# Kernel tuning notes

Hardware: AMD Instinct MI355X
Metric: run time of the kernel (lower is better)

The kernel has to match this reference:

```python
import jax, jax.numpy as jnp
import numpy as np

N, E, F, HID, HEADS, G = 20000, 320000, 64, 64, 4, 64
HC = HEADS * HID  # 256
NHID, NOUT = 256, 128
INV_SQRT2 = 0.7071067811865476


def _gat(x, src, dst, W, a_s, a_d, bias):
    # GATConv (v1), eval mode (no dropout); src/dst already include self-loops (PyG default)
    H, C = a_s.shape
    h = (x @ W).reshape(-1, H, C)  # [N,H,C]
    al_s = jnp.einsum('nhc,hc->nh', h, a_s)
    al_d = jnp.einsum('nhc,hc->nh', h, a_d)
    e = jax.nn.leaky_relu(al_s[src] + al_d[dst], 0.2)  # [Etot,H]
    m = jax.ops.segment_max(e, dst, num_segments=N)
    ex = jnp.exp(e - m[dst])
    den = jax.ops.segment_sum(ex, dst, num_segments=N)
    coef = ex / den[dst]  # softmax over incoming edges per target node
    out = jax.ops.segment_sum(h[src] * coef[:, :, None], dst, num_segments=N)
    return out.reshape(-1, H * C) + bias


def _bn(h, g, b):
    # BatchNorm1d, training-mode stats (biased var), eps=1e-5
    mu = h.mean(axis=0)
    var = h.var(axis=0)
    return g * (h - mu) * jax.lax.rsqrt(var + 1e-5) + b


def _block(x, src, dst, W1, a1s, a1d, b1, g1, be1, W2, a2s, a2d, b2, g2, be2, Wr, br, Wf, bf):
    h = jax.nn.relu(_bn(_gat(x, src, dst, W1, a1s, a1d, b1), g1, be1))
    h = jax.nn.relu(_bn(_gat(h, src, dst, W2, a2s, a2d, b2), g2, be2))
    res = x @ Wr + br
    return ((h + res) * INV_SQRT2) @ Wf + bf


def setup_inputs():
    ks = iter(jax.random.split(jax.random.key(0), 64))
    def rn(shape, scale=0.05):
        return jax.random.normal(next(ks), shape, dtype=jnp.float32) * scale
    inp = {}
    inp['x'] = jax.random.normal(next(ks), (N, F), dtype=jnp.float32)
    inp['edge_index'] = jax.random.randint(next(ks), (2, E), 0, N, dtype=jnp.int32)
    inp['batch'] = jnp.sort(jax.random.randint(next(ks), (N,), 0, G, dtype=jnp.int32))
    for b, cin in enumerate([F, HID]):
        p = 'b%d_' % b
        inp[p + 'W1'] = rn((cin, HC)); inp[p + 'a1s'] = rn((HEADS, HID)); inp[p + 'a1d'] = rn((HEADS, HID))
        inp[p + 'b1'] = jnp.zeros((HC,), jnp.float32)
        inp[p + 'g1'] = jnp.ones((HC,), jnp.float32); inp[p + 'be1'] = jnp.zeros((HC,), jnp.float32)
        inp[p + 'W2'] = rn((HC, HC)); inp[p + 'a2s'] = rn((1, HC)); inp[p + 'a2d'] = rn((1, HC))
        inp[p + 'b2'] = jnp.zeros((HC,), jnp.float32)
        inp[p + 'g2'] = jnp.ones((HC,), jnp.float32); inp[p + 'be2'] = jnp.zeros((HC,), jnp.float32)
        inp[p + 'Wr'] = rn((cin, HC)); inp[p + 'br'] = jnp.zeros((HC,), jnp.float32)
        inp[p + 'Wf'] = rn((HC, HID)); inp[p + 'bf'] = jnp.zeros((HID,), jnp.float32)
    inp['Wh1'] = rn((HID, NHID)); inp['bh1'] = jnp.zeros((NHID,), jnp.float32)
    inp['Wh2'] = rn((NHID, NOUT)); inp['bh2'] = jnp.zeros((NOUT,), jnp.float32)
    return inp


def reference(x, edge_index, batch,
              b0_W1, b0_a1s, b0_a1d, b0_b1, b0_g1, b0_be1, b0_W2, b0_a2s, b0_a2d, b0_b2, b0_g2, b0_be2, b0_Wr, b0_br, b0_Wf, b0_bf,
              b1_W1, b1_a1s, b1_a1d, b1_b1, b1_g1, b1_be1, b1_W2, b1_a2s, b1_a2d, b1_b2, b1_g2, b1_be2, b1_Wr, b1_br, b1_Wf, b1_bf,
              Wh1, bh1, Wh2, bh2):
    loops = jnp.arange(N, dtype=edge_index.dtype)
    src = jnp.concatenate([edge_index[0], loops])
    dst = jnp.concatenate([edge_index[1], loops])
    x = _block(x, src, dst, b0_W1, b0_a1s, b0_a1d, b0_b1, b0_g1, b0_be1, b0_W2, b0_a2s, b0_a2d, b0_b2, b0_g2, b0_be2, b0_Wr, b0_br, b0_Wf, b0_bf)
    x = _block(x, src, dst, b1_W1, b1_a1s, b1_a1d, b1_b1, b1_g1, b1_be1, b1_W2, b1_a2s, b1_a2d, b1_b2, b1_g2, b1_be2, b1_Wr, b1_br, b1_Wf, b1_bf)
    cnt = jax.ops.segment_sum(jnp.ones((N,), x.dtype), batch, num_segments=G)
    pooled = jax.ops.segment_sum(x, batch, num_segments=G) / jnp.maximum(cnt, 1.0)[:, None]
    h = jax.nn.relu(pooled @ Wh1 + bh1)
    return h @ Wh2 + bh2
```

## Files before the change

kernel.cpp:

```cpp
#include <hip/hip_runtime.h>

#define N_NODES 20000
#define N_EDGES 320000
#define ETOT (N_EDGES + N_NODES)
#define G_GROUPS 64


__global__ __launch_bounds__(256) void k_hist(const int* __restrict__ ei, int* __restrict__ counts) {
    int e = blockIdx.x * 256 + threadIdx.x;
    if (e >= ETOT) return;
    int dst = (e < N_EDGES) ? ei[N_EDGES + e] : (e - N_EDGES);
    atomicAdd(&counts[dst], 1);
}

__global__ __launch_bounds__(1024) void k_scan(const int* __restrict__ counts, int* __restrict__ offs,
                                               int* __restrict__ cursor) {
    __shared__ int sdata[1024];
    const int t = threadIdx.x;
    const int chunk = (N_NODES + 1023) / 1024;
    int base = t * chunk;
    int s = 0;
    for (int i = 0; i < chunk; i++) { int idx = base + i; if (idx < N_NODES) s += counts[idx]; }
    sdata[t] = s;
    __syncthreads();
    for (int off = 1; off < 1024; off <<= 1) {
        int v = (t >= off) ? sdata[t - off] : 0;
        __syncthreads();
        sdata[t] += v;
        __syncthreads();
    }
    int prefix = (t == 0) ? 0 : sdata[t - 1];
    for (int i = 0; i < chunk; i++) {
        int idx = base + i;
        if (idx < N_NODES) {
            int cv = counts[idx];
            offs[idx] = prefix;
            cursor[idx] = prefix;
            prefix += cv;
        }
    }
    if (t == 1023) offs[N_NODES] = sdata[1023];
}

__global__ __launch_bounds__(256) void k_scatter(const int* __restrict__ ei, int* __restrict__ cursor,
                                                 int* __restrict__ csr_src, int* __restrict__ csr_dst) {
    int e = blockIdx.x * 256 + threadIdx.x;
    if (e >= ETOT) return;
    int src = (e < N_EDGES) ? ei[e] : (e - N_EDGES);
    int dst = (e < N_EDGES) ? ei[N_EDGES + e] : (e - N_EDGES);
    int p = atomicAdd(&cursor[dst], 1);
    csr_src[p] = src;
    csr_dst[p] = dst;
}


template <int H>
__global__ __launch_bounds__(256) void k_edgew(const int* __restrict__ csr_src, const int* __restrict__ csr_dst,
                                               const float* __restrict__ alS, const float* __restrict__ alD,
                                               float* __restrict__ wex) {
    int p = blockIdx.x * 256 + threadIdx.x;
    if (p >= ETOT) return;
    int s = csr_src[p], d = csr_dst[p];
    if (H == 4) {
        float4 a = *(const float4*)(alS + s * 4);
        float4 b = *(const float4*)(alD + d * 4);
        float4 v = {a.x + b.x, a.y + b.y, a.z + b.z, a.w + b.w};
        v.x = (v.x > 0.f) ? v.x : 0.2f * v.x;
        v.y = (v.y > 0.f) ? v.y : 0.2f * v.y;
        v.z = (v.z > 0.f) ? v.z : 0.2f * v.z;
        v.w = (v.w > 0.f) ? v.w : 0.2f * v.w;
        float4 w = {__expf(v.x), __expf(v.y), __expf(v.z), __expf(v.w)};
        *(float4*)(wex + p * 4) = w;
    } else {
        float v = alS[s] + alD[d];
        v = (v > 0.f) ? v : 0.2f * v;
        wex[p] = __expf(v);
    }
}


__global__ __launch_bounds__(256) void k_gemm64_dual(const float* __restrict__ x, const float* __restrict__ W1,
                                                     const float* __restrict__ Wr, const float* __restrict__ br,
                                                     const float* __restrict__ a_s, const float* __restrict__ a_d,
                                                     float* __restrict__ h, float* __restrict__ res,
                                                     float* __restrict__ alS, float* __restrict__ alD) {
    const int rb = blockIdx.x >> 2, cs = blockIdx.x & 3;
    const int row0 = rb * 64;
    const int nrows = min(64, N_NODES - row0);
    const int t = threadIdx.x;
    __shared__ float xs[32 * 68];
    __shared__ float b1s[32 * 64];
    __shared__ float brs[32 * 64];
    const int lane = t & 63;
    const int c0 = (t & 15) * 4;
    const int r0 = (t >> 4) * 4;
    const int rl = (t & 15) | ((t >> 6) << 4);
    const int c4 = (t >> 4) & 3;
    float acc1[4][4] = {}, acc2[4][4] = {};
    for (int k0 = 0; k0 < 64; k0 += 32) {
        if (k0) __syncthreads();
        {
            #pragma unroll
            for (int jj = 0; jj < 2; jj++) {
                int cc = c4 + 4 * jj;
                float4 v = {0.f, 0.f, 0.f, 0.f};
                if (rl < nrows) v = *(const float4*)(x + (row0 + rl) * 64 + k0 + cc * 4);
                xs[(cc * 4 + 0) * 68 + rl] = v.x;
                xs[(cc * 4 + 1) * 68 + rl] = v.y;
                xs[(cc * 4 + 2) * 68 + rl] = v.z;
                xs[(cc * 4 + 3) * 68 + rl] = v.w;
            }
        }
        {
            int cc = (t & 15) * 4;
            int k = t >> 4;
            #pragma unroll
            for (int pass = 0; pass < 2; pass++, k += 16) {
                *(float4*)(b1s + k * 64 + cc) = *(const float4*)(W1 + (k0 + k) * 256 + cs * 64 + cc);
                *(float4*)(brs + k * 64 + cc) = *(const float4*)(Wr + (k0 + k) * 256 + cs * 64 + cc);
            }
        }
        __syncthreads();
        #pragma unroll 8
        for (int k = 0; k < 32; k++) {
            float4 av = *(const float4*)(xs + k * 68 + r0);
            float4 b1 = *(const float4*)(b1s + k * 64 + c0);
            float4 b2 = *(const float4*)(brs + k * 64 + c0);
            float a[4] = {av.x, av.y, av.z, av.w};
            #pragma unroll
            for (int i = 0; i < 4; i++) {
                acc1[i][0] += a[i] * b1.x; acc1[i][1] += a[i] * b1.y;
                acc1[i][2] += a[i] * b1.z; acc1[i][3] += a[i] * b1.w;
                acc2[i][0] += a[i] * b2.x; acc2[i][1] += a[i] * b2.y;
                acc2[i][2] += a[i] * b2.z; acc2[i][3] += a[i] * b2.w;
            }
        }
    }
    const int gcol = cs * 64 + c0;
    float4 bv = *(const float4*)(br + gcol);
    float4 asv = *(const float4*)(a_s + gcol);
    float4 adv = *(const float4*)(a_d + gcol);
    #pragma unroll
    for (int i = 0; i < 4; i++) {
        int gr = row0 + r0 + i;
        bool ok = (r0 + i) < nrows;
        float4 o1 = {acc1[i][0], acc1[i][1], acc1[i][2], acc1[i][3]};
        if (ok) {
            *(float4*)(h + gr * 256 + gcol) = o1;
            float4 o2 = {acc2[i][0] + bv.x, acc2[i][1] + bv.y, acc2[i][2] + bv.z, acc2[i][3] + bv.w};
            *(float4*)(res + gr * 256 + gcol) = o2;
        }
        float ps = o1.x * asv.x + o1.y * asv.y + o1.z * asv.z + o1.w * asv.w;
        float pd = o1.x * adv.x + o1.y * adv.y + o1.z * adv.z + o1.w * adv.w;
        #pragma unroll
        for (int off = 8; off > 0; off >>= 1) {
            ps += __shfl_down(ps, off);
            pd += __shfl_down(pd, off);
        }
        if (((lane & 15) == 0) && ok) {
            alS[gr * 4 + cs] = ps;
            alD[gr * 4 + cs] = pd;
        }
    }
}


__global__ __launch_bounds__(256) void k_alpha(const float* __restrict__ h, const float* __restrict__ a_s,
                                               const float* __restrict__ a_d, float* __restrict__ alS,
                                               float* __restrict__ alD) {
    int node = blockIdx.x * 4 + (threadIdx.x >> 6);
    int lane = threadIdx.x & 63;
    if (node >= N_NODES) return;
    const float4 hv = *(const float4*)(h + node * 256 + lane * 4);
    const float4 as = *(const float4*)(a_s + lane * 4);
    const float4 ad = *(const float4*)(a_d + lane * 4);
    float ps = hv.x * as.x + hv.y * as.y + hv.z * as.z + hv.w * as.w;
    float pd = hv.x * ad.x + hv.y * ad.y + hv.z * ad.z + hv.w * ad.w;
    #pragma unroll
    for (int off = 32; off > 0; off >>= 1) {
        ps += __shfl_down(ps, off);
        pd += __shfl_down(pd, off);
    }
    if (lane == 0) {
        alS[node] = ps;
        alD[node] = pd;
    }
}


template <int H>
__global__ __launch_bounds__(256) void k_agg(const float* __restrict__ h, const float* __restrict__ wex,
                                             const int* __restrict__ offs, const int* __restrict__ csr_src,
                                             const float* __restrict__ bias, float* __restrict__ out) {
    int node = blockIdx.x * 4 + (threadIdx.x >> 6);
    int lane = threadIdx.x & 63;
    if (node >= N_NODES) return;
    const int head = (lane * H) >> 6;
    int e0 = offs[node], e1 = offs[node + 1];
    float den = 0.f, a0 = 0.f, a1 = 0.f, a2 = 0.f, a3 = 0.f;
    int e = e0;
    for (; e + 4 <= e1; e += 4) {
        int s0 = csr_src[e], s1 = csr_src[e + 1], s2 = csr_src[e + 2], s3 = csr_src[e + 3];
        float w0 = wex[(e + 0) * H + head];
        float w1 = wex[(e + 1) * H + head];
        float w2 = wex[(e + 2) * H + head];
        float w3 = wex[(e + 3) * H + head];
        const float4 h0 = *(const float4*)(h + s0 * 256 + lane * 4);
        const float4 h1 = *(const float4*)(h + s1 * 256 + lane * 4);
        const float4 h2 = *(const float4*)(h + s2 * 256 + lane * 4);
        const float4 h3 = *(const float4*)(h + s3 * 256 + lane * 4);
        den += (w0 + w1) + (w2 + w3);
        a0 += w0 * h0.x + w1 * h1.x + w2 * h2.x + w3 * h3.x;
        a1 += w0 * h0.y + w1 * h1.y + w2 * h2.y + w3 * h3.y;
        a2 += w0 * h0.z + w1 * h1.z + w2 * h2.z + w3 * h3.z;
        a3 += w0 * h0.w + w1 * h1.w + w2 * h2.w + w3 * h3.w;
    }
    for (; e < e1; e++) {
        int s = csr_src[e];
        float w = wex[e * H + head];
        const float4 hv = *(const float4*)(h + s * 256 + lane * 4);
        den += w;
        a0 += w * hv.x; a1 += w * hv.y; a2 += w * hv.z; a3 += w * hv.w;
    }
    float inv = 1.f / den;
    const float4 bv = *(const float4*)(bias + lane * 4);
    float4 o = {a0 * inv + bv.x, a1 * inv + bv.y, a2 * inv + bv.z, a3 * inv + bv.w};
    *(float4*)(out + node * 256 + lane * 4) = o;
}


__global__ __launch_bounds__(256) void k_bnstats(const float* __restrict__ x, float* __restrict__ sum,
                                                 float* __restrict__ sumsq) {
    int c = threadIdx.x;
    float s = 0.f, q = 0.f;
    for (int r = blockIdx.x; r < N_NODES; r += gridDim.x) {
        float v = x[r * 256 + c];
        s += v; q += v * v;
    }
    atomicAdd(&sum[c], s);
    atomicAdd(&sumsq[c], q);
}

__global__ __launch_bounds__(256) void k_bnfin(const float* __restrict__ sum, const float* __restrict__ sumsq,
                                               const float* __restrict__ g, const float* __restrict__ be,
                                               float* __restrict__ scale, float* __restrict__ shift) {
    int c = threadIdx.x;
    float mu = sum[c] * (1.f / N_NODES);
    float var = sumsq[c] * (1.f / N_NODES) - mu * mu;
    float sc = g[c] * rsqrtf(var + 1e-5f);
    scale[c] = sc;
    shift[c] = be[c] - mu * sc;
}


__global__ __launch_bounds__(256) void k_gemm256(const float* __restrict__ A, const float* __restrict__ scale,
                                                 const float* __restrict__ shift, const float* __restrict__ B,
                                                 float* __restrict__ C) {
    const int rb = blockIdx.x >> 2, cs = blockIdx.x & 3;
    const int row0 = rb * 128;
    const int col0 = cs * 64;
    const int nrows = min(128, N_NODES - row0);
    const int t = threadIdx.x;
    __shared__ float xs[32 * 132];
    __shared__ float bs[32 * 64];
    __shared__ float scs[256], shs[256];
    scs[t] = scale[t];
    shs[t] = shift[t];
    const int rl = (t & 15) | ((t >> 6) << 4);
    const int c4 = (t >> 4) & 3;
    const int c0 = (t & 15) * 4;
    const int r0 = (t >> 4) * 8;
    float acc[8][4] = {};
    for (int k0 = 0; k0 < 256; k0 += 32) {
        __syncthreads();
        #pragma unroll
        for (int i = 0; i < 2; i++) {
            int r = rl + 64 * i;
            #pragma unroll
            for (int jj = 0; jj < 2; jj++) {
                int cc = c4 + 4 * jj;
                int kcol = k0 + cc * 4;
                float4 w = {0.f, 0.f, 0.f, 0.f};
                if (r < nrows) {
                    float4 v = *(const float4*)(A + (row0 + r) * 256 + kcol);
                    w.x = fmaxf(v.x * scs[kcol + 0] + shs[kcol + 0], 0.f);
                    w.y = fmaxf(v.y * scs[kcol + 1] + shs[kcol + 1], 0.f);
                    w.z = fmaxf(v.z * scs[kcol + 2] + shs[kcol + 2], 0.f);
                    w.w = fmaxf(v.w * scs[kcol + 3] + shs[kcol + 3], 0.f);
                }
                xs[(cc * 4 + 0) * 132 + r] = w.x;
                xs[(cc * 4 + 1) * 132 + r] = w.y;
                xs[(cc * 4 + 2) * 132 + r] = w.z;
                xs[(cc * 4 + 3) * 132 + r] = w.w;
            }
        }
        {
            int ccB = (t & 15) * 4;
            int kB = t >> 4;
            #pragma unroll
            for (int pass = 0; pass < 2; pass++, kB += 16) {
                *(float4*)(bs + kB * 64 + ccB) = *(const float4*)(B + (k0 + kB) * 256 + col0 + ccB);
            }
        }
        __syncthreads();
        #pragma unroll 8
        for (int k = 0; k < 32; k++) {
            float4 a0 = *(const float4*)(xs + k * 132 + r0);
            float4 a1 = *(const float4*)(xs + k * 132 + r0 + 4);
            float4 bv = *(const float4*)(bs + k * 64 + c0);
            float a[8] = {a0.x, a0.y, a0.z, a0.w, a1.x, a1.y, a1.z, a1.w};
            #pragma unroll
            for (int i = 0; i < 8; i++) {
                acc[i][0] += a[i] * bv.x; acc[i][1] += a[i] * bv.y;
                acc[i][2] += a[i] * bv.z; acc[i][3] += a[i] * bv.w;
            }
        }
    }
    #pragma unroll
    for (int i = 0; i < 8; i++) {
        if ((r0 + i) < nrows) {
            int gr = row0 + r0 + i;
            float4 o = {acc[i][0], acc[i][1], acc[i][2], acc[i][3]};
            *(float4*)(C + gr * 256 + col0 + c0) = o;
        }
    }
}


__global__ __launch_bounds__(256) void k_gemm_final(const float* __restrict__ A, const float* __restrict__ scale,
                                                    const float* __restrict__ shift, const float* __restrict__ res,
                                                    const float* __restrict__ B, const float* __restrict__ bias,
                                                    float* __restrict__ y) {
    const int row0 = blockIdx.x * 32;
    const int t = threadIdx.x;
    const float INVS = 0.70710678118654752440f;
    __shared__ float xs[32 * 36];
    __shared__ float bs[32 * 64];
    __shared__ float scs[256], shs[256];
    scs[t] = scale[t];
    shs[t] = shift[t];
    const int rf = (t & 15) | ((t >> 7) << 4);
    const int cf = (t >> 4) & 7;
    const int c0 = (t & 15) * 4;
    const int r0 = (t >> 4) * 2;
    float acc[2][4] = {};
    for (int k0 = 0; k0 < 256; k0 += 32) {
        __syncthreads();
        {
            int kcol = k0 + cf * 4;
            int gi = (row0 + rf) * 256 + kcol;
            float4 v = *(const float4*)(A + gi);
            float4 rv = *(const float4*)(res + gi);
            xs[(cf * 4 + 0) * 36 + rf] = (fmaxf(v.x * scs[kcol + 0] + shs[kcol + 0], 0.f) + rv.x) * INVS;
            xs[(cf * 4 + 1) * 36 + rf] = (fmaxf(v.y * scs[kcol + 1] + shs[kcol + 1], 0.f) + rv.y) * INVS;
            xs[(cf * 4 + 2) * 36 + rf] = (fmaxf(v.z * scs[kcol + 2] + shs[kcol + 2], 0.f) + rv.z) * INVS;
            xs[(cf * 4 + 3) * 36 + rf] = (fmaxf(v.w * scs[kcol + 3] + shs[kcol + 3], 0.f) + rv.w) * INVS;
        }
        {
            int cc = (t & 15) * 4;
            int k = t >> 4;
            #pragma unroll
            for (int pass = 0; pass < 2; pass++, k += 16) {
                *(float4*)(bs + k * 64 + cc) = *(const float4*)(B + (k0 + k) * 64 + cc);
            }
        }
        __syncthreads();
        #pragma unroll 8
        for (int k = 0; k < 32; k++) {
            float2 av = *(const float2*)(xs + k * 36 + r0);
            float4 bv = *(const float4*)(bs + k * 64 + c0);
            acc[0][0] += av.x * bv.x; acc[0][1] += av.x * bv.y;
            acc[0][2] += av.x * bv.z; acc[0][3] += av.x * bv.w;
            acc[1][0] += av.y * bv.x; acc[1][1] += av.y * bv.y;
            acc[1][2] += av.y * bv.z; acc[1][3] += av.y * bv.w;
        }
    }
    float4 bv = *(const float4*)(bias + c0);
    #pragma unroll
    for (int i = 0; i < 2; i++) {
        int gr = row0 + r0 + i;
        float4 o = {acc[i][0] + bv.x, acc[i][1] + bv.y, acc[i][2] + bv.z, acc[i][3] + bv.w};
        *(float4*)(y + gr * 64 + c0) = o;
    }
}


__global__ __launch_bounds__(256) void k_pool_head(const float* __restrict__ x, const int* __restrict__ batch,
                                                   const float* __restrict__ Wh1, const float* __restrict__ bh1,
                                                   const float* __restrict__ Wh2, const float* __restrict__ bh2,
                                                   float* __restrict__ out) {
    const int g = blockIdx.x;
    const int t = threadIdx.x;
    int lo = 0, hi = N_NODES;
    while (lo < hi) { int mid = (lo + hi) >> 1; if (batch[mid] < g) lo = mid + 1; else hi = mid; }
    int start = lo;
    hi = N_NODES;
    while (lo < hi) { int mid = (lo + hi) >> 1; if (batch[mid] < g + 1) lo = mid + 1; else hi = mid; }
    int end = lo;
    float cnt = (float)(end - start);

    __shared__ float part[256];
    __shared__ float p[64];
    __shared__ float hrow[256];
    const int c = t & 63;
    float s = 0.f;
    for (int r = start + (t >> 6); r < end; r += 4) s += x[r * 64 + c];
    part[t] = s;
    __syncthreads();
    if (t < 64) {
        float v = part[t] + part[t + 64] + part[t + 128] + part[t + 192];
        p[t] = v / fmaxf(cnt, 1.f);
    }
    __syncthreads();
    float a = bh1[t];
    #pragma unroll 8
    for (int k = 0; k < 64; k++) a += p[k] * Wh1[k * 256 + t];
    hrow[t] = fmaxf(a, 0.f);
    __syncthreads();
    if (t < 128) {
        float o = bh2[t];
        #pragma unroll 8
        for (int k = 0; k < 256; k++) o += hrow[k] * Wh2[k * 128 + t];
        out[g * 128 + t] = o;
    }
}


extern "C" void kernel_launch(void* const* d_in, const int* in_sizes, int n_in,
                              void* d_out, int out_size, void* d_ws, size_t ws_size,
                              hipStream_t stream) {
    (void)in_sizes; (void)n_in; (void)out_size; (void)ws_size;
    const float* x0 = (const float*)d_in[0];
    const int* ei = (const int*)d_in[1];
    const int* batch = (const int*)d_in[2];
    const float* Wh1 = (const float*)d_in[35];
    const float* bh1 = (const float*)d_in[36];
    const float* Wh2 = (const float*)d_in[37];
    const float* bh2 = (const float*)d_in[38];

    char* p = (char*)d_ws;
    auto alloc = [&](size_t bytes) -> void* {
        void* r = (void*)p;
        p += (bytes + 255) & ~(size_t)255;
        return r;
    };
    int* counts = (int*)alloc((size_t)N_NODES * 4);
    int* offs = (int*)alloc((size_t)(N_NODES + 1) * 4);
    int* cursor = (int*)alloc((size_t)N_NODES * 4);
    int* csr_src = (int*)alloc((size_t)ETOT * 4);
    int* csr_dst = (int*)alloc((size_t)ETOT * 4);
    float* wex = (float*)alloc((size_t)ETOT * 4 * 4);
    float* alS = (float*)alloc((size_t)N_NODES * 4 * 4);
    float* alD = (float*)alloc((size_t)N_NODES * 4 * 4);
    float* bnsum = (float*)alloc(2048);
    float* bnsq = bnsum + 256;
    float* scaleb = (float*)alloc(1024);
    float* shiftb = (float*)alloc(1024);
    float* hbuf = (float*)alloc((size_t)N_NODES * 256 * 4);
    float* obuf = (float*)alloc((size_t)N_NODES * 256 * 4);
    float* rbuf = (float*)alloc((size_t)N_NODES * 256 * 4);
    float* xout = (float*)alloc((size_t)N_NODES * 64 * 4);

    hipMemsetAsync(counts, 0, (size_t)N_NODES * 4, stream);
    k_hist<<<(ETOT + 255) / 256, 256, 0, stream>>>(ei, counts);
    k_scan<<<1, 1024, 0, stream>>>(counts, offs, cursor);
    k_scatter<<<(ETOT + 255) / 256, 256, 0, stream>>>(ei, cursor, csr_src, csr_dst);

    const int tile64_blocks = ((N_NODES + 63) / 64) * 4;
    const int tile128_blocks = ((N_NODES + 127) / 128) * 4;
    const int node_blocks = (N_NODES + 3) / 4;
    const int edge_blocks = (ETOT + 255) / 256;
    const int final_blocks = N_NODES / 32;

    auto run_block = [&](const float* xin, int base) {
        const float* W1 = (const float*)d_in[base + 0];
        const float* a1s = (const float*)d_in[base + 1];
        const float* a1d = (const float*)d_in[base + 2];
        const float* b1 = (const float*)d_in[base + 3];
        const float* g1 = (const float*)d_in[base + 4];
        const float* be1 = (const float*)d_in[base + 5];
        const float* W2 = (const float*)d_in[base + 6];
        const float* a2s = (const float*)d_in[base + 7];
        const float* a2d = (const float*)d_in[base + 8];
        const float* b2 = (const float*)d_in[base + 9];
        const float* g2 = (const float*)d_in[base + 10];
        const float* be2 = (const float*)d_in[base + 11];
        const float* Wr = (const float*)d_in[base + 12];
        const float* br = (const float*)d_in[base + 13];
        const float* Wf = (const float*)d_in[base + 14];
        const float* bf = (const float*)d_in[base + 15];

        k_gemm64_dual<<<tile64_blocks, 256, 0, stream>>>(xin, W1, Wr, br, a1s, a1d, hbuf, rbuf, alS, alD);
        k_edgew<4><<<edge_blocks, 256, 0, stream>>>(csr_src, csr_dst, alS, alD, wex);
        k_agg<4><<<node_blocks, 256, 0, stream>>>(hbuf, wex, offs, csr_src, b1, obuf);
        hipMemsetAsync(bnsum, 0, 2048, stream);
        k_bnstats<<<256, 256, 0, stream>>>(obuf, bnsum, bnsq);
        k_bnfin<<<1, 256, 0, stream>>>(bnsum, bnsq, g1, be1, scaleb, shiftb);
        k_gemm256<<<tile128_blocks, 256, 0, stream>>>(obuf, scaleb, shiftb, W2, hbuf);
        k_alpha<<<node_blocks, 256, 0, stream>>>(hbuf, a2s, a2d, alS, alD);
        k_edgew<1><<<edge_blocks, 256, 0, stream>>>(csr_src, csr_dst, alS, alD, wex);
        k_agg<1><<<node_blocks, 256, 0, stream>>>(hbuf, wex, offs, csr_src, b2, obuf);
        hipMemsetAsync(bnsum, 0, 2048, stream);
        k_bnstats<<<256, 256, 0, stream>>>(obuf, bnsum, bnsq);
        k_bnfin<<<1, 256, 0, stream>>>(bnsum, bnsq, g2, be2, scaleb, shiftb);
        k_gemm_final<<<final_blocks, 256, 0, stream>>>(obuf, scaleb, shiftb, rbuf, Wf, bf, xout);
    };

    run_block(x0, 3);
    run_block(xout, 19);

    k_pool_head<<<G_GROUPS, 256, 0, stream>>>(xout, batch, Wh1, bh1, Wh2, bh2, (float*)d_out);
}
```

Measured before the change: 738.7 us.

## Fuse edge softmax weights into aggregation and alpha into second GEMM

Attention edge weights are now computed inside the aggregation kernel from per-node alpha values, which removes the separate edge-weight kernels, the wex buffer and csr_dst. The second-layer alpha dot products are folded into the 256-wide GEMM epilogue as per-column-slice partials, summed by a small reduction kernel, so the standalone alpha kernel goes away. That GEMM's row tile drops from 128 to 64, and the BN accumulators are zeroed by k_bnfin and the initial memset instead of per-layer memsets. The aggregation loop is unrolled by 8 edges, at the cost of extra exp work and alpha gathers per lane.

New measurement: 705.7 us. 1.05x faster.

```diff
diff --git a/kernel.cpp b/kernel.cpp
--- a/kernel.cpp
+++ b/kernel.cpp
@@ -43,39 +43,13 @@
 }
 
 __global__ __launch_bounds__(256) void k_scatter(const int* __restrict__ ei, int* __restrict__ cursor,
-                                                 int* __restrict__ csr_src, int* __restrict__ csr_dst) {
+                                                 int* __restrict__ csr_src) {
     int e = blockIdx.x * 256 + threadIdx.x;
     if (e >= ETOT) return;
     int src = (e < N_EDGES) ? ei[e] : (e - N_EDGES);
     int dst = (e < N_EDGES) ? ei[N_EDGES + e] : (e - N_EDGES);
     int p = atomicAdd(&cursor[dst], 1);
     csr_src[p] = src;
-    csr_dst[p] = dst;
-}
-
-
-template <int H>
-__global__ __launch_bounds__(256) void k_edgew(const int* __restrict__ csr_src, const int* __restrict__ csr_dst,
-                                               const float* __restrict__ alS, const float* __restrict__ alD,
-                                               float* __restrict__ wex) {
-    int p = blockIdx.x * 256 + threadIdx.x;
-    if (p >= ETOT) return;
-    int s = csr_src[p], d = csr_dst[p];
-    if (H == 4) {
-        float4 a = *(const float4*)(alS + s * 4);
-        float4 b = *(const float4*)(alD + d * 4);
-        float4 v = {a.x + b.x, a.y + b.y, a.z + b.z, a.w + b.w};
-        v.x = (v.x > 0.f) ? v.x : 0.2f * v.x;
-        v.y = (v.y > 0.f) ? v.y : 0.2f * v.y;
-        v.z = (v.z > 0.f) ? v.z : 0.2f * v.z;
-        v.w = (v.w > 0.f) ? v.w : 0.2f * v.w;
-        float4 w = {__expf(v.x), __expf(v.y), __expf(v.z), __expf(v.w)};
-        *(float4*)(wex + p * 4) = w;
-    } else {
-        float v = alS[s] + alD[d];
-        v = (v > 0.f) ? v : 0.2f * v;
-        wex[p] = __expf(v);
-    }
 }
 
 
@@ -165,60 +139,47 @@
 }
 
 
-__global__ __launch_bounds__(256) void k_alpha(const float* __restrict__ h, const float* __restrict__ a_s,
-                                               const float* __restrict__ a_d, float* __restrict__ alS,
-                                               float* __restrict__ alD) {
+template <int H>
+__global__ __launch_bounds__(256) void k_agg(const float* __restrict__ h, const float* __restrict__ alS,
+                                             const float* __restrict__ alD, const int* __restrict__ offs,
+                                             const int* __restrict__ csr_src, const float* __restrict__ bias,
+                                             float* __restrict__ out) {
     int node = blockIdx.x * 4 + (threadIdx.x >> 6);
     int lane = threadIdx.x & 63;
     if (node >= N_NODES) return;
-    const float4 hv = *(const float4*)(h + node * 256 + lane * 4);
-    const float4 as = *(const float4*)(a_s + lane * 4);
-    const float4 ad = *(const float4*)(a_d + lane * 4);
-    float ps = hv.x * as.x + hv.y * as.y + hv.z * as.z + hv.w * as.w;
-    float pd = hv.x * ad.x + hv.y * ad.y + hv.z * ad.z + hv.w * ad.w;
-    #pragma unroll
-    for (int off = 32; off > 0; off >>= 1) {
-        ps += __shfl_down(ps, off);
-        pd += __shfl_down(pd, off);
-    }
-    if (lane == 0) {
-        alS[node] = ps;
-        alD[node] = pd;
-    }
-}
-
-
-template <int H>
-__global__ __launch_bounds__(256) void k_agg(const float* __restrict__ h, const float* __restrict__ wex,
-                                             const int* __restrict__ offs, const int* __restrict__ csr_src,
-                                             const float* __restrict__ bias, float* __restrict__ out) {
-    int node = blockIdx.x * 4 + (threadIdx.x >> 6);
-    int lane = threadIdx.x & 63;
-    if (node >= N_NODES) return;
-    const int head = (lane * H) >> 6;
+    const int head = (H == 4) ? (lane >> 4) : 0;
+    const float ald = alD[node * H + head];
     int e0 = offs[node], e1 = offs[node + 1];
+    const float* hp = h + lane * 4;
     float den = 0.f, a0 = 0.f, a1 = 0.f, a2 = 0.f, a3 = 0.f;
     int e = e0;
-    for (; e + 4 <= e1; e += 4) {
-        int s0 = csr_src[e], s1 = csr_src[e + 1], s2 = csr_src[e + 2], s3 = csr_src[e + 3];
-        float w0 = wex[(e + 0) * H + head];
-        float w1 = wex[(e + 1) * H + head];
-        float w2 = wex[(e + 2) * H + head];
-        float w3 = wex[(e + 3) * H + head];
-        const float4 h0 = *(const float4*)(h + s0 * 256 + lane * 4);
-        const float4 h1 = *(const float4*)(h + s1 * 256 + lane * 4);
-        const float4 h2 = *(const float4*)(h + s2 * 256 + lane * 4);
-        const float4 h3 = *(const float4*)(h + s3 * 256 + lane * 4);
-        den += (w0 + w1) + (w2 + w3);
-        a0 += w0 * h0.x + w1 * h1.x + w2 * h2.x + w3 * h3.x;
-        a1 += w0 * h0.y + w1 * h1.y + w2 * h2.y + w3 * h3.y;
-        a2 += w0 * h0.z + w1 * h1.z + w2 * h2.z + w3 * h3.z;
-        a3 += w0 * h0.w + w1 * h1.w + w2 * h2.w + w3 * h3.w;
+    for (; e + 8 <= e1; e += 8) {
+        int s[8];
+        #pragma unroll
+        for (int i = 0; i < 8; i++) s[i] = csr_src[e + i];
+        float4 hv[8];
+        #pragma unroll
+        for (int i = 0; i < 8; i++) hv[i] = *(const float4*)(hp + s[i] * 256);
+        float w[8];
+        #pragma unroll
+        for (int i = 0; i < 8; i++) {
+            float v = alS[s[i] * H + head] + ald;
+            v = (v > 0.f) ? v : 0.2f * v;
+            w[i] = __expf(v);
+        }
+        #pragma unroll
+        for (int i = 0; i < 8; i++) {
+            den += w[i];
+            a0 += w[i] * hv[i].x; a1 += w[i] * hv[i].y;
+            a2 += w[i] * hv[i].z; a3 += w[i] * hv[i].w;
+        }
     }
     for (; e < e1; e++) {
         int s = csr_src[e];
-        float w = wex[e * H + head];
-        const float4 hv = *(const float4*)(h + s * 256 + lane * 4);
+        float v = alS[s * H + head] + ald;
+        v = (v > 0.f) ? v : 0.2f * v;
+        float w = __expf(v);
+        const float4 hv = *(const float4*)(hp + s * 256);
         den += w;
         a0 += w * hv.x; a1 += w * hv.y; a2 += w * hv.z; a3 += w * hv.w;
     }
@@ -241,7 +202,7 @@
     atomicAdd(&sumsq[c], q);
 }
 
-__global__ __launch_bounds__(256) void k_bnfin(const float* __restrict__ sum, const float* __restrict__ sumsq,
+__global__ __launch_bounds__(256) void k_bnfin(float* __restrict__ sum, float* __restrict__ sumsq,
                                                const float* __restrict__ g, const float* __restrict__ be,
                                                float* __restrict__ scale, float* __restrict__ shift) {
     int c = threadIdx.x;
@@ -250,48 +211,51 @@
     float sc = g[c] * rsqrtf(var + 1e-5f);
     scale[c] = sc;
     shift[c] = be[c] - mu * sc;
+    sum[c] = 0.f;
+    sumsq[c] = 0.f;
 }
 
 
 __global__ __launch_bounds__(256) void k_gemm256(const float* __restrict__ A, const float* __restrict__ scale,
                                                  const float* __restrict__ shift, const float* __restrict__ B,
-                                                 float* __restrict__ C) {
+                                                 const float* __restrict__ a_s, const float* __restrict__ a_d,
+                                                 float* __restrict__ C, float* __restrict__ alSp,
+                                                 float* __restrict__ alDp) {
     const int rb = blockIdx.x >> 2, cs = blockIdx.x & 3;
-    const int row0 = rb * 128;
+    const int row0 = rb * 64;
     const int col0 = cs * 64;
-    const int nrows = min(128, N_NODES - row0);
+    const int nrows = min(64, N_NODES - row0);
     const int t = threadIdx.x;
-    __shared__ float xs[32 * 132];
+    __shared__ float xs[32 * 68];
     __shared__ float bs[32 * 64];
     __shared__ float scs[256], shs[256];
     scs[t] = scale[t];
     shs[t] = shift[t];
+    const int lane = t & 63;
     const int rl = (t & 15) | ((t >> 6) << 4);
     const int c4 = (t >> 4) & 3;
     const int c0 = (t & 15) * 4;
-    const int r0 = (t >> 4) * 8;
-    float acc[8][4] = {};
+    const int r0 = (t >> 4) * 4;
+    float acc[4][4] = {};
     for (int k0 = 0; k0 < 256; k0 += 32) {
         __syncthreads();
-        #pragma unroll
-        for (int i = 0; i < 2; i++) {
-            int r = rl + 64 * i;
+        {
             #pragma unroll
             for (int jj = 0; jj < 2; jj++) {
                 int cc = c4 + 4 * jj;
                 int kcol = k0 + cc * 4;
                 float4 w = {0.f, 0.f, 0.f, 0.f};
-                if (r < nrows) {
-                    float4 v = *(const float4*)(A + (row0 + r) * 256 + kcol);
+                if (rl < nrows) {
+                    float4 v = *(const float4*)(A + (row0 + rl) * 256 + kcol);
                     w.x = fmaxf(v.x * scs[kcol + 0] + shs[kcol + 0], 0.f);
                     w.y = fmaxf(v.y * scs[kcol + 1] + shs[kcol + 1], 0.f);
                     w.z = fmaxf(v.z * scs[kcol + 2] + shs[kcol + 2], 0.f);
                     w.w = fmaxf(v.w * scs[kcol + 3] + shs[kcol + 3], 0.f);
                 }
-                xs[(cc * 4 + 0) * 132 + r] = w.x;
-                xs[(cc * 4 + 1) * 132 + r] = w.y;
-                xs[(cc * 4 + 2) * 132 + r] = w.z;
-                xs[(cc * 4 + 3) * 132 + r] = w.w;
+                xs[(cc * 4 + 0) * 68 + rl] = w.x;
+                xs[(cc * 4 + 1) * 68 + rl] = w.y;
+                xs[(cc * 4 + 2) * 68 + rl] = w.z;
+                xs[(cc * 4 + 3) * 68 + rl] = w.w;
             }
         }
         {
@@ -305,25 +269,44 @@
         __syncthreads();
         #pragma unroll 8
         for (int k = 0; k < 32; k++) {
-            float4 a0 = *(const float4*)(xs + k * 132 + r0);
-            float4 a1 = *(const float4*)(xs + k * 132 + r0 + 4);
+            float4 av = *(const float4*)(xs + k * 68 + r0);
             float4 bv = *(const float4*)(bs + k * 64 + c0);
-            float a[8] = {a0.x, a0.y, a0.z, a0.w, a1.x, a1.y, a1.z, a1.w};
-            #pragma unroll
-            for (int i = 0; i < 8; i++) {
+            float a[4] = {av.x, av.y, av.z, av.w};
+            #pragma unroll
+            for (int i = 0; i < 4; i++) {
                 acc[i][0] += a[i] * bv.x; acc[i][1] += a[i] * bv.y;
                 acc[i][2] += a[i] * bv.z; acc[i][3] += a[i] * bv.w;
             }
         }
     }
+    float4 asv = *(const float4*)(a_s + col0 + c0);
+    float4 adv = *(const float4*)(a_d + col0 + c0);
     #pragma unroll
-    for (int i = 0; i < 8; i++) {
-        if ((r0 + i) < nrows) {
-            int gr = row0 + r0 + i;
-            float4 o = {acc[i][0], acc[i][1], acc[i][2], acc[i][3]};
-            *(float4*)(C + gr * 256 + col0 + c0) = o;
-        }
-    }
+    for (int i = 0; i < 4; i++) {
+        int gr = row0 + r0 + i;
+        bool ok = (r0 + i) < nrows;
+        float4 o = {acc[i][0], acc[i][1], acc[i][2], acc[i][3]};
+        if (ok) *(float4*)(C + gr * 256 + col0 + c0) = o;
+        float ps = o.x * asv.x + o.y * asv.y + o.z * asv.z + o.w * asv.w;
+        float pd = o.x * adv.x + o.y * adv.y + o.z * adv.z + o.w * adv.w;
+        #pragma unroll
+        for (int off = 8; off > 0; off >>= 1) {
+            ps += __shfl_down(ps, off);
+            pd += __shfl_down(pd, off);
+        }
+        if (((lane & 15) == 0) && ok) {
+            alSp[cs * N_NODES + gr] = ps;
+            alDp[cs * N_NODES + gr] = pd;
+        }
+    }
+}
+
+__global__ __launch_bounds__(256) void k_alred(const float* __restrict__ alSp, const float* __restrict__ alDp,
+                                               float* __restrict__ alS, float* __restrict__ alD) {
+    int n = blockIdx.x * 256 + threadIdx.x;
+    if (n >= N_NODES) return;
+    alS[n] = (alSp[n] + alSp[N_NODES + n]) + (alSp[2 * N_NODES + n] + alSp[3 * N_NODES + n]);
+    alD[n] = (alDp[n] + alDp[N_NODES + n]) + (alDp[2 * N_NODES + n] + alDp[3 * N_NODES + n]);
 }
 
 
@@ -445,15 +428,16 @@
         return r;
     };
     int* counts = (int*)alloc((size_t)N_NODES * 4);
+    float* bnsum = (float*)alloc(2048);
+    float* bnsq = bnsum + 256;
+    const size_t zero_bytes = (((size_t)N_NODES * 4 + 255) & ~(size_t)255) + 2048;
     int* offs = (int*)alloc((size_t)(N_NODES + 1) * 4);
     int* cursor = (int*)alloc((size_t)N_NODES * 4);
     int* csr_src = (int*)alloc((size_t)ETOT * 4);
-    int* csr_dst = (int*)alloc((size_t)ETOT * 4);
-    float* wex = (float*)alloc((size_t)ETOT * 4 * 4);
     float* alS = (float*)alloc((size_t)N_NODES * 4 * 4);
     float* alD = (float*)alloc((size_t)N_NODES * 4 * 4);
-    float* bnsum = (float*)alloc(2048);
-    float* bnsq = bnsum + 256;
+    float* alSp = (float*)alloc((size_t)N_NODES * 4 * 4);
+    float* alDp = (float*)alloc((size_t)N_NODES * 4 * 4);
     float* scaleb = (float*)alloc(1024);
     float* shiftb = (float*)alloc(1024);
     float* hbuf = (float*)alloc((size_t)N_NODES * 256 * 4);
@@ -461,15 +445,14 @@
     float* rbuf = (float*)alloc((size_t)N_NODES * 256 * 4);
     float* xout = (float*)alloc((size_t)N_NODES * 64 * 4);
 
-    hipMemsetAsync(counts, 0, (size_t)N_NODES * 4, stream);
+    hipMemsetAsync(counts, 0, zero_bytes, stream);
     k_hist<<<(ETOT + 255) / 256, 256, 0, stream>>>(ei, counts);
     k_scan<<<1, 1024, 0, stream>>>(counts, offs, cursor);
-    k_scatter<<<(ETOT + 255) / 256, 256, 0, stream>>>(ei, cursor, csr_src, csr_dst);
+    k_scatter<<<(ETOT + 255) / 256, 256, 0, stream>>>(ei, cursor, csr_src);
 
     const int tile64_blocks = ((N_NODES + 63) / 64) * 4;
-    const int tile128_blocks = ((N_NODES + 127) / 128) * 4;
     const int node_blocks = (N_NODES + 3) / 4;
-    const int edge_blocks = (ETOT + 255) / 256;
+    const int red_blocks = (N_NODES + 255) / 256;
     const int final_blocks = N_NODES / 32;
 
     auto run_block = [&](const float* xin, int base) {
@@ -491,16 +474,12 @@
         const float* bf = (const float*)d_in[base + 15];
 
         k_gemm64_dual<<<tile64_blocks, 256, 0, stream>>>(xin, W1, Wr, br, a1s, a1d, hbuf, rbuf, alS, alD);
-        k_edgew<4><<<edge_blocks, 256, 0, stream>>>(csr_src, csr_dst, alS, alD, wex);
-        k_agg<4><<<node_blocks, 256, 0, stream>>>(hbuf, wex, offs, csr_src, b1, obuf);
-        hipMemsetAsync(bnsum, 0, 2048, stream);
+        k_agg<4><<<node_blocks, 256, 0, stream>>>(hbuf, alS, alD, offs, csr_src, b1, obuf);
         k_bnstats<<<256, 256, 0, stream>>>(obuf, bnsum, bnsq);
         k_bnfin<<<1, 256, 0, stream>>>(bnsum, bnsq, g1, be1, scaleb, shiftb);
-        k_gemm256<<<tile128_blocks, 256, 0, stream>>>(obuf, scaleb, shiftb, W2, hbuf);
-        k_alpha<<<node_blocks, 256, 0, stream>>>(hbuf, a2s, a2d, alS, alD);
-        k_edgew<1><<<edge_blocks, 256, 0, stream>>>(csr_src, csr_dst, alS, alD, wex);
-        k_agg<1><<<node_blocks, 256, 0, stream>>>(hbuf, wex, offs, csr_src, b2, obuf);
-        hipMemsetAsync(bnsum, 0, 2048, stream);
+        k_gemm256<<<tile64_blocks, 256, 0, stream>>>(obuf, scaleb, shiftb, W2, a2s, a2d, hbuf, alSp, alDp);
+        k_alred<<<red_blocks, 256, 0, stream>>>(alSp, alDp, alS, alD);
+        k_agg<1><<<node_blocks, 256, 0, stream>>>(hbuf, alS, alD, offs, csr_src, b2, obuf);
         k_bnstats<<<256, 256, 0, stream>>>(obuf, bnsum, bnsq);
         k_bnfin<<<1, 256, 0, stream>>>(bnsum, bnsq, g2, be2, scaleb, shiftb);
         k_gemm_final<<<final_blocks, 256, 0, stream>>>(obuf, scaleb, shiftb, rbuf, Wf, bf, xout);
```
